# Optimization experiments

Measured on AMD Instinct MI355X. Metric: run time of the kernel, lower is better.

Reference implementation:

```python
import jax, jax.numpy as jnp
import numpy as np

SRC_V, TGT_V, EMB, ENC_H, DEC_H = 36616, 23262, 300, 512, 1024
T_SRC, T_TGT, B = 50, 50, 64


def setup_inputs():
    key = jax.random.key(0)
    ks = jax.random.split(key, 24)
    p = lambda k, s: jax.random.normal(k, s, dtype=jnp.float32) * 0.05
    return {
        'train_src_batch': jax.random.randint(ks[0], (T_SRC, B), 0, SRC_V),
        'train_trg_batch': jax.random.randint(ks[1], (T_TGT, B), 0, TGT_V),
        'enc_Wih_f': p(ks[2], (4 * ENC_H, EMB)), 'enc_Whh_f': p(ks[3], (4 * ENC_H, ENC_H)),
        'enc_bih_f': p(ks[4], (4 * ENC_H,)), 'enc_bhh_f': p(ks[5], (4 * ENC_H,)),
        'enc_Wih_r': p(ks[6], (4 * ENC_H, EMB)), 'enc_Whh_r': p(ks[7], (4 * ENC_H, ENC_H)),
        'enc_bih_r': p(ks[8], (4 * ENC_H,)), 'enc_bhh_r': p(ks[9], (4 * ENC_H,)),
        'dec_Wih': p(ks[10], (4 * DEC_H, DEC_H + EMB)), 'dec_Whh': p(ks[11], (4 * DEC_H, DEC_H)),
        'dec_bih': p(ks[12], (4 * DEC_H,)), 'dec_bhh': p(ks[13], (4 * DEC_H,)),
        'enc_emb': p(ks[14], (SRC_V, EMB)), 'dec_emb': p(ks[15], (TGT_V, EMB)),
        'wi': p(ks[16], (DEC_H, DEC_H)), 'wo': p(ks[17], (DEC_H, 2 * DEC_H)),
        'gen_w': p(ks[18], (TGT_V, DEC_H)), 'gen_b': p(ks[19], (TGT_V,)),
    }


def _lstm_update(gates, c):
    # PyTorch gate order: i, f, g, o
    i, f, g, o = jnp.split(gates, 4, axis=-1)
    c = jax.nn.sigmoid(f) * c + jax.nn.sigmoid(i) * jnp.tanh(g)
    h = jax.nn.sigmoid(o) * jnp.tanh(c)
    return h, c


def _run_lstm(x, Wih, Whh, bih, bhh, H):
    # x: [T, B, E]; precompute input projection for all timesteps
    xp = jnp.einsum('tbe,ge->tbg', x, Wih) + bih + bhh
    b = x.shape[1]
    def step(carry, xpt):
        h, c = carry
        h, c = _lstm_update(xpt + h @ Whh.T, c)
        return (h, c), h
    init = (jnp.zeros((b, H), x.dtype), jnp.zeros((b, H), x.dtype))
    (hT, cT), hs = jax.lax.scan(step, init, xp)
    return hs, hT, cT


def _forward(train_src_batch, train_trg_batch, enc_Wih_f, enc_Whh_f, enc_bih_f, enc_bhh_f,
             enc_Wih_r, enc_Whh_r, enc_bih_r, enc_bhh_r, dec_Wih, dec_Whh, dec_bih, dec_bhh,
             enc_emb, dec_emb, wi, wo, gen_w, gen_b):
    x = enc_emb[train_src_batch]                       # [T_src, B, 300]
    hs_f, hT_f, cT_f = _run_lstm(x, enc_Wih_f, enc_Whh_f, enc_bih_f, enc_bhh_f, ENC_H)
    hs_r, hT_r, cT_r = _run_lstm(x[::-1], enc_Wih_r, enc_Whh_r, enc_bih_r, enc_bhh_r, ENC_H)
    enc_out = jnp.concatenate([hs_f, hs_r[::-1]], axis=-1)  # [T_src, B, 1024]
    b = x.shape[1]
    # h.permute(1,2,0).view(B,1024): interleave fwd/bwd along last axis
    h0 = jnp.stack([hT_f, hT_r], axis=-1).reshape(b, DEC_H)
    c0 = jnp.stack([cT_f, cT_r], axis=-1).reshape(b, DEC_H)
    prev_emb = dec_emb[train_trg_batch[:-1]]           # teacher forcing: [T_tgt-1, B, 300]

    def dec_step(carry, pe):
        h, c = carry
        q = h @ wi.T                                   # [B, 1024]
        score = jnp.einsum('tbh,bh->tb', enc_out, q)   # [T_src, B]
        attn = jax.nn.softmax(score, axis=0)           # softmax over source time
        st = jnp.einsum('tb,tbh->bh', attn, enc_out)   # [B, 1024]
        ct = jnp.tanh(jnp.concatenate([st, h], axis=1) @ wo.T)
        inp = jnp.concatenate([ct, pe], axis=1)        # [B, 1324]
        gates = inp @ dec_Wih.T + h @ dec_Whh.T + dec_bih + dec_bhh
        h, c = _lstm_update(gates, c)
        logp = jax.nn.log_softmax(h @ gen_w.T + gen_b, axis=-1)
        return (h, c), logp

    _, outs = jax.lax.scan(dec_step, (h0, c0), prev_emb)  # [T_tgt-1, B, V]
    result = jnp.concatenate([jnp.zeros((1, b, TGT_V), outs.dtype), outs], axis=0)
    return result


def reference(train_src_batch, train_trg_batch, enc_Wih_f, enc_Whh_f, enc_bih_f, enc_bhh_f,
              enc_Wih_r, enc_Whh_r, enc_bih_r, enc_bhh_r, dec_Wih, dec_Whh, dec_bih, dec_bhh,
              enc_emb, dec_emb, wi, wo, gen_w, gen_b):
    return _forward(train_src_batch, train_trg_batch, enc_Wih_f, enc_Whh_f, enc_bih_f, enc_bhh_f,
                    enc_Wih_r, enc_Whh_r, enc_bih_r, enc_bhh_r, dec_Wih, dec_Whh, dec_bih, dec_bhh,
                    enc_emb, dec_emb, wi, wo, gen_w, gen_b)
```

## Files before the change

kernel.cpp:

```cpp
#include <hip/hip_runtime.h>
#include <cstdint>
#include <cmath>

#define NB    64
#define EMBD  300
#define EMBP  320
#define EH    512
#define DH    1024
#define GV    23262
#define GVP   23296
#define TSRC  50
#define TDEC  49
#define LDS_SCR 131072
#define LDS_TOT (131072 + 16384 + 256)
#define LDS_ENC (65536 + 16384 + 256)
#define FS    32

typedef __attribute__((ext_vector_type(8))) _Float16 f16x8;
typedef __attribute__((ext_vector_type(4))) float f32x4;

__device__ __forceinline__ float sigm(float x){ return 1.f/(1.f+expf(-x)); }

__device__ __forceinline__ void cohS16(_Float16* p, _Float16 v){
  union { _Float16 f; unsigned short u; } c; c.f = v;
  __hip_atomic_store((unsigned short*)p, c.u, __ATOMIC_RELAXED, __HIP_MEMORY_SCOPE_AGENT);
}
__device__ __forceinline__ void cohS32(float* p, float v){
  __hip_atomic_store(p, v, __ATOMIC_RELAXED, __HIP_MEMORY_SCOPE_AGENT);
}
__device__ __forceinline__ void cohS64(void* p, unsigned long long v){
  __hip_atomic_store((unsigned long long*)p, v, __ATOMIC_RELAXED, __HIP_MEMORY_SCOPE_AGENT);
}
__device__ __forceinline__ void cohS32u(void* p, unsigned int v){
  __hip_atomic_store((unsigned int*)p, v, __ATOMIC_RELAXED, __HIP_MEMORY_SCOPE_AGENT);
}
__device__ __forceinline__ unsigned short h2u(float f){
  union { _Float16 h; unsigned short u; } c; c.h = (_Float16)f; return c.u;
}
__device__ __forceinline__ unsigned long long pk4h(float a, float b, float c, float d){
  return (unsigned long long)h2u(a) | ((unsigned long long)h2u(b)<<16)
       | ((unsigned long long)h2u(c)<<32) | ((unsigned long long)h2u(d)<<48);
}
__device__ __forceinline__ unsigned int pk2h(float a, float b){
  return (unsigned int)h2u(a) | ((unsigned int)h2u(b)<<16);
}
__device__ __forceinline__ unsigned long long pk2f(float a, float b){
  union { float f; unsigned int u; } x, y; x.f = a; y.f = b;
  return (unsigned long long)x.u | ((unsigned long long)y.u<<32);
}

__device__ __forceinline__ int ldF(int* p){
  return __hip_atomic_load(p, __ATOMIC_RELAXED, __HIP_MEMORY_SCOPE_AGENT);
}
__device__ __forceinline__ void stF(int* p, int v){
  __hip_atomic_store(p, v, __ATOMIC_RELAXED, __HIP_MEMORY_SCOPE_AGENT);
}
__device__ __forceinline__ void post(int* flagArr, int idx, int epoch){
  __syncthreads();
  if (threadIdx.x == 0) stF(flagArr + idx*FS, epoch);
}
__device__ __forceinline__ void flagWaitIdx(int* flagArr, int myIdx, bool active, int epoch)
{
  if (active) {
    int* p = flagArr + myIdx*FS;
    while (ldF(p) < epoch) __builtin_amdgcn_s_sleep(1);
  }
  __syncthreads();
  __atomic_signal_fence(__ATOMIC_SEQ_CST);
}

__device__ __forceinline__ void stageW(char* dst, const _Float16* __restrict__ src,
                                       int srcld, int nrows, int ncols, int tid)
{
  const int nch = ncols >> 3;
  for (int i = tid; i < nrows*nch; i += 256) {
    int row = i / nch, c = i - row*nch;
    *(f16x8*)(dst + row*ncols*2 + ((c*16) ^ ((row&7)<<4))) =
        *(const f16x8*)(src + (size_t)row*srcld + c*8);
  }
}

template<int K>
__device__ __forceinline__ void mm16L(f32x4 (&acc)[4],
    const _Float16* __restrict__ A, int lda,
    const char* ldsB, int rowbytes, int koffB, int lane)
{
  const int r = lane & 15, q = lane >> 4;
  const _Float16* a0 = A + r*lda + q*8;
  const char* b0 = ldsB + r*rowbytes + koffB;
  const int sw = (r & 7) << 4;
#pragma unroll
  for (int g = 0; g < K/256; ++g) {
    f16x8 av[8][4], bv[8];
#pragma unroll
    for (int s = 0; s < 8; ++s) {
      int sl = g*8 + s;
      bv[s] = *(const f16x8*)(b0 + ((sl*64 + q*16) ^ sw));
#pragma unroll
      for (int m = 0; m < 4; ++m)
        av[s][m] = *(const f16x8*)(a0 + m*16*lda + sl*32);
    }
#pragma unroll
    for (int s = 0; s < 8; ++s)
#pragma unroll
      for (int m = 0; m < 4; ++m)
        acc[m] = __builtin_amdgcn_mfma_f32_16x16x32_f16(av[s][m], bv[s], acc[m], 0, 0, 0);
  }
}

__global__ void cvt16s(const float* __restrict__ src, _Float16* __restrict__ dst,
                       int rows, int sld, int scols, int dcols)
{
  int idx = blockIdx.x*256 + threadIdx.x;
  if (idx >= rows*dcols) return;
  int c = idx % dcols, rr = idx / dcols;
  dst[idx] = (c < scols) ? (_Float16)src[(size_t)rr*sld + c] : (_Float16)0.f;
}

__global__ void cvt16t(const float* __restrict__ src, _Float16* __restrict__ dst, int n)
{
  int idx = blockIdx.x*256 + threadIdx.x;
  if (idx >= n*n) return;
  int rr = idx / n, c = idx - rr*n;
  dst[(size_t)c*n + rr] = (_Float16)src[idx];
}

__global__ void addb(const float* __restrict__ a, const float* __restrict__ b,
                     float* __restrict__ o, int n)
{
  int i = blockIdx.x*256 + threadIdx.x;
  if (i < n) o[i] = a[i] + b[i];
}

__global__ void k_embed(const int* __restrict__ src, const int* __restrict__ trg,
                        const float* __restrict__ eemb, const float* __restrict__ demb,
                        _Float16* __restrict__ x_h, _Float16* __restrict__ xrev_h,
                        _Float16* __restrict__ pe_h)
{
  int idx = blockIdx.x*256 + threadIdx.x;
  const int tot1 = TSRC*NB*EMBP;
  const int tot2 = TDEC*NB*EMBP;
  if (idx < tot1) {
    int e = idx % EMBP, rb = idx / EMBP;
    int t = rb >> 6, b = rb & 63;
    float v = 0.f;
    if (e < EMBD) v = eemb[(size_t)src[rb]*EMBD + e];
    _Float16 hv = (_Float16)v;
    x_h[idx] = hv;
    xrev_h[(size_t)((TSRC-1-t)*NB + b)*EMBP + e] = hv;
  } else if (idx < tot1 + tot2) {
    int k = idx - tot1;
    int e = k % EMBP, rb = k / EMBP;
    float v = 0.f;
    if (e < EMBD) v = demb[(size_t)trg[rb]*EMBD + e];
    pe_h[k] = (_Float16)v;
  }
}

__device__ __forceinline__ void swz_block(int& m0, int& n0)
{
  int nwg = gridDim.x*gridDim.y;
  int flat = blockIdx.y*gridDim.x + blockIdx.x;
  int q = nwg >> 3, rr = nwg & 7;
  int xcd = flat & 7, pos = flat >> 3;
  int wg = (xcd < rr) ? xcd*(q+1) + pos : rr*(q+1) + (xcd-rr)*q + pos;
  m0 = (wg / gridDim.x) * 128;
  n0 = (wg % gridDim.x) * 128;
}

__global__ __launch_bounds__(256) void gemm128(
    const _Float16* __restrict__ A, int lda,
    const _Float16* __restrict__ W, int ldw,
    const float* __restrict__ bias,
    float* __restrict__ out, int ldo,
    int K, int mvalid, int nvalid, int rowoff)
{
  __shared__ _Float16 As[128*64];
  __shared__ _Float16 Bs[128*64];
  const int tid = threadIdx.x;
  int m0, n0;
  swz_block(m0, n0);
  const int w = tid >> 6, lane = tid & 63, r = lane & 15, q = lane >> 4;
  const int mw = (w >> 1)*64, nw = (w & 1)*64;
  f32x4 acc[4][4];
#pragma unroll
  for (int mi=0; mi<4; ++mi)
#pragma unroll
    for (int ni=0; ni<4; ++ni) acc[mi][ni] = 0.f;

  for (int kt = 0; kt < K; kt += 64) {
    f16x8 ra[4], rb[4];
#pragma unroll
    for (int j = 0; j < 4; ++j) {
      int c = j*256 + tid, row = c >> 3, cc = c & 7;
      ra[j] = *(const f16x8*)(A + (size_t)(m0+row)*lda + kt + cc*8);
      rb[j] = *(const f16x8*)(W + (size_t)(n0+row)*ldw + kt + cc*8);
    }
    __syncthreads();
#pragma unroll
    for (int j = 0; j < 4; ++j) {
      int c = j*256 + tid, row = c >> 3, cc = c & 7;
      int sw = cc ^ (row & 7);
      *(f16x8*)((char*)As + row*128 + (sw<<4)) = ra[j];
      *(f16x8*)((char*)Bs + row*128 + (sw<<4)) = rb[j];
    }
    __syncthreads();
#pragma unroll
    for (int kk = 0; kk < 64; kk += 32) {
      int ch = (kk >> 3) + q;
      f16x8 av[4], bv[4];
#pragma unroll
      for (int mi=0; mi<4; ++mi) {
        int row = mw + mi*16 + r;
        av[mi] = *(const f16x8*)((char*)As + row*128 + ((ch ^ (row&7))<<4));
      }
#pragma unroll
      for (int ni=0; ni<4; ++ni) {
        int row = nw + ni*16 + r;
        bv[ni] = *(const f16x8*)((char*)Bs + row*128 + ((ch ^ (row&7))<<4));
      }
#pragma unroll
      for (int mi=0; mi<4; ++mi)
#pragma unroll
        for (int ni=0; ni<4; ++ni)
          acc[mi][ni] = __builtin_amdgcn_mfma_f32_16x16x32_f16(av[mi], bv[ni], acc[mi][ni], 0,0,0);
    }
  }
#pragma unroll
  for (int mi=0; mi<4; ++mi)
#pragma unroll
    for (int ni=0; ni<4; ++ni)
#pragma unroll
      for (int e=0; e<4; ++e) {
        int mrow = m0 + mw + mi*16 + q*4 + e;
        int col  = n0 + nw + ni*16 + r;
        if (mrow < mvalid && col < nvalid)
          out[(size_t)(mrow + rowoff)*ldo + col] = acc[mi][ni][e] + bias[col];
      }
}

__global__ __launch_bounds__(256) void gemm128h(
    const _Float16* __restrict__ A, int lda,
    const _Float16* __restrict__ W, int ldw,
    const float* __restrict__ bias,
    _Float16* __restrict__ out, int ldo,
    int K, int mvalid, int nvalid)
{
  __shared__ _Float16 As[128*64];
  __shared__ _Float16 Bs[128*64];
  const int tid = threadIdx.x;
  int m0, n0;
  swz_block(m0, n0);
  const int w = tid >> 6, lane = tid & 63, r = lane & 15, q = lane >> 4;
  const int mw = (w >> 1)*64, nw = (w & 1)*64;
  f32x4 acc[4][4];
#pragma unroll
  for (int mi=0; mi<4; ++mi)
#pragma unroll
    for (int ni=0; ni<4; ++ni) acc[mi][ni] = 0.f;

  for (int kt = 0; kt < K; kt += 64) {
    f16x8 ra[4], rb[4];
#pragma unroll
    for (int j = 0; j < 4; ++j) {
      int c = j*256 + tid, row = c >> 3, cc = c & 7;
      ra[j] = *(const f16x8*)(A + (size_t)(m0+row)*lda + kt + cc*8);
      rb[j] = *(const f16x8*)(W + (size_t)(n0+row)*ldw + kt + cc*8);
    }
    __syncthreads();
#pragma unroll
    for (int j = 0; j < 4; ++j) {
      int c = j*256 + tid, row = c >> 3, cc = c & 7;
      int sw = cc ^ (row & 7);
      *(f16x8*)((char*)As + row*128 + (sw<<4)) = ra[j];
      *(f16x8*)((char*)Bs + row*128 + (sw<<4)) = rb[j];
    }
    __syncthreads();
#pragma unroll
    for (int kk = 0; kk < 64; kk += 32) {
      int ch = (kk >> 3) + q;
      f16x8 av[4], bv[4];
#pragma unroll
      for (int mi=0; mi<4; ++mi) {
        int row = mw + mi*16 + r;
        av[mi] = *(const f16x8*)((char*)As + row*128 + ((ch ^ (row&7))<<4));
      }
#pragma unroll
      for (int ni=0; ni<4; ++ni) {
        int row = nw + ni*16 + r;
        bv[ni] = *(const f16x8*)((char*)Bs + row*128 + ((ch ^ (row&7))<<4));
      }
#pragma unroll
      for (int mi=0; mi<4; ++mi)
#pragma unroll
        for (int ni=0; ni<4; ++ni)
          acc[mi][ni] = __builtin_amdgcn_mfma_f32_16x16x32_f16(av[mi], bv[ni], acc[mi][ni], 0,0,0);
    }
  }
#pragma unroll
  for (int mi=0; mi<4; ++mi)
#pragma unroll
    for (int ni=0; ni<4; ++ni)
#pragma unroll
      for (int e=0; e<4; ++e) {
        int mrow = m0 + mw + mi*16 + q*4 + e;
        int col  = n0 + nw + ni*16 + r;
        if (mrow < mvalid && col < nvalid)
          out[(size_t)mrow*ldo + col] = (_Float16)(acc[mi][ni][e] + bias[col]);
      }
}

struct EA {
  const _Float16 *whhF, *whhR;
  const float *xpF, *xpR;
  _Float16 *h;
  _Float16 *enc_out;
  _Float16 *dh0;
  float *dc;
  int *flags;
};

__global__ __launch_bounds__(256, 1) void enc_seq(EA a)
{
  extern __shared__ char lds[];
  const int tid = threadIdx.x, w = tid >> 6, lane = tid & 63;
  const int wgid = blockIdx.x;
  const int r = lane & 15, q4 = lane >> 4;
  float (*sm4)[64][16] = (float(*)[64][16])(lds + 65536);

  const int dir = wgid >> 5, j0 = (wgid & 31) << 4;
  const _Float16* whh = dir ? a.whhR : a.whhF;
  for (int g = 0; g < 4; ++g)
    stageW(lds + g*16384, whh + (size_t)(g*EH + j0)*EH, EH, 16, 512, tid);
  __syncthreads();

  const int b = tid >> 2, jq = (tid & 3) * 4;
  float creg[4] = {0.f, 0.f, 0.f, 0.f};
  const float* xpbase = dir ? a.xpR : a.xpF;

  for (int t = 0; t < TSRC; ++t) {
    float xr[4][4];
#pragma unroll
    for (int g = 0; g < 4; ++g)
#pragma unroll
      for (int k = 0; k < 4; ++k)
        xr[g][k] = xpbase[((size_t)t*NB + b)*2048 + g*EH + j0 + jq + k];
    if (t) flagWaitIdx(a.flags, dir*32 + tid, tid < 32, t);
    const _Float16* H = a.h + ((size_t)(TSRC-t)*2 + dir)*NB*EH;
    f32x4 acc[4];
#pragma unroll
    for (int m=0;m<4;++m) acc[m] = 0.f;
    mm16L<EH>(acc, H, EH, lds + w*16384, 1024, 0, lane);
#pragma unroll
    for (int m=0;m<4;++m)
#pragma unroll
      for (int e=0;e<4;++e) sm4[w][m*16 + q4*4 + e][r] = acc[m][e];
    __syncthreads();
    _Float16* Ho = a.h + ((size_t)(TSRC-1-t)*2 + dir)*NB*EH;
    const int erow = dir ? (TSRC-1 - t) : t;
    float hv[4];
#pragma unroll
    for (int k = 0; k < 4; ++k) {
      int jj = jq + k;
      float gi = sm4[0][b][jj] + xr[0][k];
      float gf = sm4[1][b][jj] + xr[1][k];
      float gg = sm4[2][b][jj] + xr[2][k];
      float go = sm4[3][b][jj] + xr[3][k];
      float cn = sigm(gf)*creg[k] + sigm(gi)*tanhf(gg);
      creg[k] = cn;
      hv[k] = sigm(go)*tanhf(cn);
    }
    cohS64(Ho + b*EH + j0 + jq, pk4h(hv[0],hv[1],hv[2],hv[3]));
    cohS64(a.enc_out + ((size_t)erow*NB + b)*DH + dir*EH + j0 + jq, pk4h(hv[0],hv[1],hv[2],hv[3]));
    if (t == TSRC-1) {
#pragma unroll
      for (int k = 0; k < 4; ++k) {
        int j = j0 + jq + k;
        cohS16(a.dh0 + b*DH + 2*j + dir, (_Float16)hv[k]);
        cohS32(a.dc + b*DH + 2*j + dir, creg[k]);
      }
    }
    post(a.flags, wgid, t+1);
  }
}

struct DA {
  const _Float16 *wo;
  const _Float16 *wdh;
  const _Float16 *w3c;
  const _Float16 *eq;
  const _Float16 *eo2;
  const _Float16 *pp;
  _Float16 *dh;
  float *dc;
  _Float16 *ct;
  float *wdd;
  _Float16 *hdec;
  int *flags;
};

__global__ __launch_bounds__(256, 1) void dec_seq(DA a)
{
  extern __shared__ char lds[];
  const int tid = threadIdx.x, w = tid >> 6, lane = tid & 63;
  const int wgid = blockIdx.x;
  const int r = lane & 15, q4 = lane >> 4;
  float (*sm4)[64][16] = (float(*)[64][16])(lds + LDS_SCR);
  float* qs = (float*)(lds + LDS_SCR);
  float* sc = (float*)(lds + LDS_SCR + 16384);

  int* FB  = a.flags;
  int* FCP = FB + 64*FS;
  int* FD  = FCP + 32*FS;

  if (wgid >= 64 && wgid < 96) {
    stageW(lds, a.wo + (size_t)((wgid-64)*32)*2048 + 1024, 2048, 32, 1024, tid);
  } else if (wgid >= 96) {
    int i = wgid - 96;
    for (int g = 0; g < 4; ++g)
      stageW(lds + g*8*2048, a.wdh + (size_t)(g*1024 + i*8)*DH, DH, 8, 1024, tid);
    for (int g = 0; g < 4; ++g)
      stageW(lds + 65536 + g*8*2048, a.w3c + (size_t)(g*1024 + i*8)*DH, DH, 8, 1024, tid);
  }
  __syncthreads();

  const bool isP2 = (wgid < 64);
  const bool isC  = (wgid >= 64 && wgid < 96);
  const bool isD  = (wgid >= 96);
  float dcreg[2] = {0.f, 0.f};

  for (int t = 0; t < TDEC; ++t) {
    const size_t cur = (size_t)(TDEC - t)*NB*DH;
    const size_t nxt = (size_t)(TDEC - 1 - t)*NB*DH;
    const _Float16* dhC = a.dh + cur;

    if (isC) {
      if (t) flagWaitIdx(FD, tid, tid < 128, t);
      const int col0 = (wgid - 64)*32;
      const int cs = w >> 1, kh = w & 1;
      f32x4 acc[4];
#pragma unroll
      for (int m=0;m<4;++m) acc[m] = 0.f;
      mm16L<512>(acc, dhC + kh*512, DH, lds + cs*16*2048, 2048, kh*1024, lane);
#pragma unroll
      for (int m=0;m<4;++m)
#pragma unroll
        for (int e=0;e<4;++e) sm4[w][m*16 + q4*4 + e][r] = acc[m][e];
      __syncthreads();
      for (int p = tid; p < 2048; p += 256) {
        int b = p >> 5, cc = p & 31;
        float v1, v2;
        int c1 = (cc & 30);
        v1 = sm4[((c1)>>4)*2][b][(c1)&15] + sm4[((c1)>>4)*2+1][b][(c1)&15];
        v2 = sm4[((c1+1)>>4)*2][b][(c1+1)&15] + sm4[((c1+1)>>4)*2+1][b][(c1+1)&15];
        if ((cc & 1) == 0)
          cohS64(a.wdd + cur + b*DH + col0 + c1, pk2f(v1, v2));
      }
      post(FCP, wgid - 64, t+1);
    }

    if (isP2) {
      if (t) flagWaitIdx(FD, tid, tid < 128, t);
      const int b = wgid;
      if (tid < 128) {
        f16x8 v = *(const f16x8*)(dhC + b*DH + tid*8);
#pragma unroll
        for (int k = 0; k < 8; ++k) qs[tid*8 + k] = (float)v[k];
      }
      __syncthreads();
      for (int tt = w; tt < TSRC; tt += 4) {
        const _Float16* er = a.eq + ((size_t)tt*NB + b)*DH + lane*16;
        const float* qq = qs + lane*16;
        f16x8 e0 = *(const f16x8*)(er);
        f16x8 e1 = *(const f16x8*)(er + 8);
        float s = 0.f;
#pragma unroll
        for (int ii=0; ii<8; ++ii) s += (float)e0[ii]*qq[ii];
#pragma unroll
        for (int ii=0; ii<8; ++ii) s += (float)e1[ii]*qq[8+ii];
#pragma unroll
        for (int o=32; o; o>>=1) s += __shfl_xor(s, o);
        if (lane == 0) sc[tt] = s;
      }
      __syncthreads();
      float mx = -1e30f;
      for (int tt=0; tt<TSRC; ++tt) mx = fmaxf(mx, sc[tt]);
      __syncthreads();
      if (tid < TSRC) sc[tid] = expf(sc[tid] - mx);
      __syncthreads();
      float s50 = 0.f;
      for (int tt=0; tt<TSRC; ++tt) s50 += sc[tt];
      const float inv = 1.f/s50;
      const int c0 = tid*4;
      float a0=0.f, a1=0.f, a2=0.f, a3=0.f;
      for (int tt=0; tt<TSRC; ++tt) {
        float wt = sc[tt];
        const _Float16* er = a.eo2 + ((size_t)tt*NB + b)*DH + c0;
        a0 += wt*(float)er[0]; a1 += wt*(float)er[1];
        a2 += wt*(float)er[2]; a3 += wt*(float)er[3];
      }
      flagWaitIdx(FCP, tid, tid < 32, t+1);
      f32x4 wd = *(const f32x4*)(a.wdd + cur + b*DH + c0);
      float v0 = tanhf(a0*inv + wd[0]);
      float v1 = tanhf(a1*inv + wd[1]);
      float v2 = tanhf(a2*inv + wd[2]);
      float v3 = tanhf(a3*inv + wd[3]);
      cohS64(a.ct + cur + b*DH + c0, pk4h(v0, v1, v2, v3));
      post(FB, wgid, t+1);
    }

    if (isD) {
      const int i = wgid - 96;
      if (t) flagWaitIdx(FD, tid, tid < 128, t);
      const int b = tid >> 2, j0 = i*8, jj2 = (tid & 3)*2;
      if (t == 0) {
        dcreg[0] = a.dc[b*DH + j0 + jj2];
        dcreg[1] = a.dc[b*DH + j0 + jj2 + 1];
      }
      const int cs = w >> 1, kh = w & 1;
      f32x4 acc[4];
#pragma unroll
      for (int m=0;m<4;++m) acc[m] = 0.f;
      mm16L<512>(acc, dhC + kh*512, DH, lds + cs*16*2048, 2048, kh*1024, lane);
      float ppv[4][2];
#pragma unroll
      for (int g = 0; g < 4; ++g)
#pragma unroll
        for (int k = 0; k < 2; ++k)
          ppv[g][k] = (float)a.pp[((size_t)t*NB + b)*4096 + g*DH + j0 + jj2 + k];
      flagWaitIdx(FB, tid, tid < 64, t+1);
      mm16L<512>(acc, a.ct + cur + kh*512, DH, lds + 65536 + cs*16*2048, 2048, kh*1024, lane);
#pragma unroll
      for (int m=0;m<4;++m)
#pragma unroll
        for (int e=0;e<4;++e) sm4[w][m*16 + q4*4 + e][r] = acc[m][e];
      __syncthreads();
      float hv[2];
#pragma unroll
      for (int k = 0; k < 2; ++k) {
        int jj = jj2 + k;
        float gi = sm4[0][b][jj]   + sm4[1][b][jj]   + ppv[0][k];
        float gf = sm4[0][b][8+jj] + sm4[1][b][8+jj] + ppv[1][k];
        float gg = sm4[2][b][jj]   + sm4[3][b][jj]   + ppv[2][k];
        float go = sm4[2][b][8+jj] + sm4[3][b][8+jj] + ppv[3][k];
        float cn = sigm(gf)*dcreg[k] + sigm(gi)*tanhf(gg);
        dcreg[k] = cn;
        hv[k] = sigm(go)*tanhf(cn);
      }
      cohS32u(a.dh + nxt + b*DH + j0 + jj2, pk2h(hv[0], hv[1]));
      post(FD, i, t+1);
      *(unsigned int*)(a.hdec + ((size_t)t*NB + b)*DH + j0 + jj2) = pk2h(hv[0], hv[1]);
    }
  }
}

__global__ __launch_bounds__(256) void lsm(float* __restrict__ out)
{
  const int row = NB + blockIdx.x;
  float* p = out + (size_t)row*GV;
  const int tid = threadIdx.x;
  __shared__ float rm[4], rl[4];
  float m = -1e30f, l = 0.f;
  for (int i = tid; i < GV; i += 256) {
    float v = p[i];
    float M = fmaxf(m, v);
    l = l*expf(m - M) + expf(v - M);
    m = M;
  }
  for (int off=32; off; off>>=1) {
    float m2 = __shfl_down(m, off), l2 = __shfl_down(l, off);
    float M = fmaxf(m, m2);
    l = l*expf(m - M) + l2*expf(m2 - M);
    m = M;
  }
  if ((tid & 63) == 0) { rm[tid>>6] = m; rl[tid>>6] = l; }
  __syncthreads();
  m = rm[0]; l = rl[0];
#pragma unroll
  for (int k=1; k<4; ++k) {
    float M = fmaxf(m, rm[k]);
    l = l*expf(m - M) + rl[k]*expf(rm[k] - M);
    m = M;
  }
  float lse = m + logf(l);
  for (int i = tid; i < GV; i += 256) p[i] -= lse;
}

extern "C" void kernel_launch(void* const* d_in, const int* in_sizes, int n_in,
                              void* d_out, int out_size, void* d_ws, size_t ws_size,
                              hipStream_t stream)
{
  const int*   src  = (const int*)d_in[0];
  const int*   trg  = (const int*)d_in[1];
  const float* WihF = (const float*)d_in[2];
  const float* WhhF = (const float*)d_in[3];
  const float* bihF = (const float*)d_in[4];
  const float* bhhF = (const float*)d_in[5];
  const float* WihR = (const float*)d_in[6];
  const float* WhhR = (const float*)d_in[7];
  const float* bihR = (const float*)d_in[8];
  const float* bhhR = (const float*)d_in[9];
  const float* dWih = (const float*)d_in[10];
  const float* dWhh = (const float*)d_in[11];
  const float* dbih = (const float*)d_in[12];
  const float* dbhh = (const float*)d_in[13];
  const float* eemb = (const float*)d_in[14];
  const float* demb = (const float*)d_in[15];
  const float* wi   = (const float*)d_in[16];
  const float* wo   = (const float*)d_in[17];
  const float* genw = (const float*)d_in[18];
  const float* genb = (const float*)d_in[19];
  float* out = (float*)d_out;

  char* ws = (char*)d_ws;
  size_t off = 0;
  auto alloc = [&](size_t bytes)->char* {
    char* p = ws + off; off = (off + bytes + 255) & ~(size_t)255; return p;
  };
  _Float16* x_h    = (_Float16*)alloc((size_t)TSRC*NB*EMBP*2);
  _Float16* xrev_h = (_Float16*)alloc((size_t)TSRC*NB*EMBP*2);
  _Float16* pe_h   = (_Float16*)alloc((size_t)TDEC*NB*EMBP*2);
  _Float16* wihF_h = (_Float16*)alloc((size_t)2048*EMBP*2);
  _Float16* wihR_h = (_Float16*)alloc((size_t)2048*EMBP*2);
  _Float16* whhF_h = (_Float16*)alloc((size_t)2048*EH*2);
  _Float16* whhR_h = (_Float16*)alloc((size_t)2048*EH*2);
  _Float16* wdh_h  = (_Float16*)alloc((size_t)4096*DH*2);
  _Float16* wo_h   = (_Float16*)alloc((size_t)DH*2048*2);
  _Float16* w3c    = (_Float16*)alloc((size_t)4096*DH*2);
  _Float16* w3pe   = (_Float16*)alloc((size_t)4096*EMBP*2);
  _Float16* wiT_h  = (_Float16*)alloc((size_t)DH*DH*2);
  _Float16* genw_h = (_Float16*)alloc((size_t)GVP*DH*2);
  float* b4f   = (float*)alloc(2048*4);
  float* b4r   = (float*)alloc(2048*4);
  float* db4   = (float*)alloc(4096*4);
  float* zb    = (float*)alloc(DH*4);
  float* xp_f  = (float*)alloc((size_t)TSRC*NB*2048*4);
  float* xp_r  = (float*)alloc((size_t)TSRC*NB*2048*4);
  _Float16* peproj = (_Float16*)alloc((size_t)TDEC*NB*4096*2);
  _Float16* enc_out = (_Float16*)alloc((size_t)TSRC*NB*DH*2);
  _Float16* eq_h  = (_Float16*)alloc((size_t)TSRC*NB*DH*2);
  _Float16* eo2_h = (_Float16*)alloc((size_t)TSRC*NB*DH*2);
  _Float16* hbuf = (_Float16*)alloc((size_t)(TSRC+1)*2*NB*EH*2);
  _Float16* dh = (_Float16*)alloc((size_t)(TDEC+1)*NB*DH*2);
  float* dc = (float*)alloc((size_t)NB*DH*4);
  _Float16* ct = (_Float16*)alloc((size_t)(TDEC+1)*NB*DH*2);
  float* wdd = (float*)alloc((size_t)(TDEC+1)*NB*DH*4);
  _Float16* hdec = (_Float16*)alloc((size_t)3200*DH*2);
  int* eflags = (int*)alloc(64*FS*4);
  int* dflags = (int*)alloc(224*FS*4);
  (void)in_sizes; (void)n_in; (void)out_size; (void)ws_size;

  hipMemsetAsync(hbuf + (size_t)TSRC*2*NB*EH, 0, (size_t)2*NB*EH*2, stream);
  hipMemsetAsync(hdec + (size_t)3136*DH, 0, (size_t)64*DH*2, stream);
  hipMemsetAsync(genw_h + (size_t)GV*DH, 0, (size_t)(GVP-GV)*DH*2, stream);
  hipMemsetAsync(out, 0, (size_t)NB*GV*4, stream);
  hipMemsetAsync(zb, 0, DH*4, stream);
  hipMemsetAsync(eflags, 0, 64*FS*4, stream);
  hipMemsetAsync(dflags, 0, 224*FS*4, stream);

  auto cgrid = [](size_t n){ return dim3((unsigned)((n + 255)/256)); };

  cvt16s<<<cgrid((size_t)2048*EMBP),256,0,stream>>>(WihF, wihF_h, 2048, EMBD, EMBD, EMBP);
  cvt16s<<<cgrid((size_t)2048*EMBP),256,0,stream>>>(WihR, wihR_h, 2048, EMBD, EMBD, EMBP);
  cvt16s<<<cgrid((size_t)2048*EH),256,0,stream>>>(WhhF, whhF_h, 2048, EH, EH, EH);
  cvt16s<<<cgrid((size_t)2048*EH),256,0,stream>>>(WhhR, whhR_h, 2048, EH, EH, EH);
  cvt16s<<<cgrid((size_t)4096*DH),256,0,stream>>>(dWhh, wdh_h, 4096, DH, DH, DH);
  cvt16s<<<cgrid((size_t)DH*2048),256,0,stream>>>(wo, wo_h, DH, 2048, 2048, 2048);
  cvt16s<<<cgrid((size_t)4096*DH),256,0,stream>>>(dWih, w3c, 4096, 1324, 1024, 1024);
  cvt16s<<<cgrid((size_t)4096*EMBP),256,0,stream>>>(dWih + 1024, w3pe, 4096, 1324, 300, EMBP);
  cvt16t<<<cgrid((size_t)DH*DH),256,0,stream>>>(wi, wiT_h, DH);
  cvt16s<<<cgrid((size_t)GV*DH),256,0,stream>>>(genw, genw_h, GV, DH, DH, DH);
  addb<<<cgrid(2048),256,0,stream>>>(bihF, bhhF, b4f, 2048);
  addb<<<cgrid(2048),256,0,stream>>>(bihR, bhhR, b4r, 2048);
  addb<<<cgrid(4096),256,0,stream>>>(dbih, dbhh, db4, 4096);
  k_embed<<<cgrid((size_t)(TSRC+TDEC)*NB*EMBP),256,0,stream>>>(src, trg, eemb, demb, x_h, xrev_h, pe_h);

  gemm128<<<dim3(16,25),256,0,stream>>>(x_h,    EMBP, wihF_h, EMBP, b4f, xp_f, 2048, EMBP, 3200, 2048, 0);
  gemm128<<<dim3(16,25),256,0,stream>>>(xrev_h, EMBP, wihR_h, EMBP, b4r, xp_r, 2048, EMBP, 3200, 2048, 0);
  gemm128h<<<dim3(32,25),256,0,stream>>>(pe_h, EMBP, w3pe, EMBP, db4, peproj, 4096, EMBP, 3136, 4096);

  EA ea;
  ea.whhF = whhF_h; ea.whhR = whhR_h;
  ea.xpF = xp_f; ea.xpR = xp_r;
  ea.h = hbuf; ea.enc_out = enc_out;
  ea.dh0 = dh + (size_t)TDEC*NB*DH;
  ea.dc = dc;
  ea.flags = eflags;
  hipFuncSetAttribute((const void*)enc_seq,
                      hipFuncAttributeMaxDynamicSharedMemorySize, LDS_ENC);
  enc_seq<<<dim3(64), 256, LDS_ENC, stream>>>(ea);

  gemm128h<<<dim3(8,25),256,0,stream>>>(enc_out, DH, wiT_h, DH, zb, eq_h, DH, DH, 3200, DH);
  gemm128h<<<dim3(8,25),256,0,stream>>>(enc_out, DH, wo_h, 2048, zb, eo2_h, DH, DH, 3200, DH);

  DA da;
  da.wo = wo_h; da.wdh = wdh_h; da.w3c = w3c;
  da.eq = eq_h; da.eo2 = eo2_h;
  da.pp = peproj;
  da.dh = dh; da.dc = dc;
  da.ct = ct; da.wdd = wdd;
  da.hdec = hdec;
  da.flags = dflags;
  hipFuncSetAttribute((const void*)dec_seq,
                      hipFuncAttributeMaxDynamicSharedMemorySize, LDS_TOT);
  dec_seq<<<dim3(224), 256, LDS_TOT, stream>>>(da);

  gemm128<<<dim3(GVP/128,25),256,0,stream>>>(hdec, DH, genw_h, DH, genb, out, GV, DH, 3136, GV, NB);
  lsm<<<3136,256,0,stream>>>(out);
}
```

Before: 2.255 ms.

## Fuse log-softmax row stats into generator GEMM and use direct global-to-LDS loads

The generator GEMM epilogue now computes a per-row online max and sum-exp over each 128-column tile and writes them to a small stats buffer. The log-softmax kernel then merges 182 partial stats per row instead of re-reading the full 23262-wide logits row to find them, which removes one full pass over the logits. Separately, both GEMM kernels stage A and W tiles with global_load_lds (buffer-to-LDS) instead of going through registers, and add an extra barrier per k-step. The epilogue adds extra exp work and shuffles in the GEMM.

```diff
diff --git a/kernel.cpp b/kernel.cpp
--- a/kernel.cpp
+++ b/kernel.cpp
@@ -9,6 +9,7 @@
 #define DH    1024
 #define GV    23262
 #define GVP   23296
+#define NCB   182
 #define TSRC  50
 #define TDEC  49
 #define LDS_SCR 131072
@@ -18,6 +19,9 @@
 
 typedef __attribute__((ext_vector_type(8))) _Float16 f16x8;
 typedef __attribute__((ext_vector_type(4))) float f32x4;
+
+typedef __attribute__((address_space(1))) const void gas_t;
+typedef __attribute__((address_space(3))) void las_t;
 
 __device__ __forceinline__ float sigm(float x){ return 1.f/(1.f+expf(-x)); }
 
@@ -168,12 +172,31 @@
   n0 = (wg % gridDim.x) * 128;
 }
 
+__device__ __forceinline__ void stage_glds(const _Float16* __restrict__ A, int lda, int m0,
+                                           const _Float16* __restrict__ W, int ldw, int n0,
+                                           int kt, char* As, char* Bs, int tid)
+{
+#pragma unroll
+  for (int j = 0; j < 4; ++j) {
+    int idx = j*256 + tid;
+    int row = idx >> 3, cc = idx & 7;
+    int sc = cc ^ (row & 7);
+    __builtin_amdgcn_global_load_lds(
+        (gas_t*)(A + (size_t)(m0+row)*lda + kt + sc*8),
+        (las_t*)(As + (j*256 + (tid & 0xffc0))*16), 16, 0, 0);
+    __builtin_amdgcn_global_load_lds(
+        (gas_t*)(W + (size_t)(n0+row)*ldw + kt + sc*8),
+        (las_t*)(Bs + (j*256 + (tid & 0xffc0))*16), 16, 0, 0);
+  }
+}
+
 __global__ __launch_bounds__(256) void gemm128(
     const _Float16* __restrict__ A, int lda,
     const _Float16* __restrict__ W, int ldw,
     const float* __restrict__ bias,
     float* __restrict__ out, int ldo,
-    int K, int mvalid, int nvalid, int rowoff)
+    int K, int mvalid, int nvalid, int rowoff,
+    float* __restrict__ gstats)
 {
   __shared__ _Float16 As[128*64];
   __shared__ _Float16 Bs[128*64];
@@ -189,21 +212,7 @@
     for (int ni=0; ni<4; ++ni) acc[mi][ni] = 0.f;
 
   for (int kt = 0; kt < K; kt += 64) {
-    f16x8 ra[4], rb[4];
-#pragma unroll
-    for (int j = 0; j < 4; ++j) {
-      int c = j*256 + tid, row = c >> 3, cc = c & 7;
-      ra[j] = *(const f16x8*)(A + (size_t)(m0+row)*lda + kt + cc*8);
-      rb[j] = *(const f16x8*)(W + (size_t)(n0+row)*ldw + kt + cc*8);
-    }
-    __syncthreads();
-#pragma unroll
-    for (int j = 0; j < 4; ++j) {
-      int c = j*256 + tid, row = c >> 3, cc = c & 7;
-      int sw = cc ^ (row & 7);
-      *(f16x8*)((char*)As + row*128 + (sw<<4)) = ra[j];
-      *(f16x8*)((char*)Bs + row*128 + (sw<<4)) = rb[j];
-    }
+    stage_glds(A, lda, m0, W, ldw, n0, kt, (char*)As, (char*)Bs, tid);
     __syncthreads();
 #pragma unroll
     for (int kk = 0; kk < 64; kk += 32) {
@@ -225,6 +234,7 @@
         for (int ni=0; ni<4; ++ni)
           acc[mi][ni] = __builtin_amdgcn_mfma_f32_16x16x32_f16(av[mi], bv[ni], acc[mi][ni], 0,0,0);
     }
+    __syncthreads();
   }
 #pragma unroll
   for (int mi=0; mi<4; ++mi)
@@ -237,6 +247,66 @@
         if (mrow < mvalid && col < nvalid)
           out[(size_t)(mrow + rowoff)*ldo + col] = acc[mi][ni][e] + bias[col];
       }
+
+  if (gstats) {
+    float pm[4][4], pl[4][4];
+#pragma unroll
+    for (int mi=0;mi<4;++mi)
+#pragma unroll
+      for (int e=0;e<4;++e){ pm[mi][e] = -1e30f; pl[mi][e] = 0.f; }
+#pragma unroll
+    for (int mi=0;mi<4;++mi)
+#pragma unroll
+      for (int ni=0;ni<4;++ni)
+#pragma unroll
+        for (int e=0;e<4;++e) {
+          int col = n0 + nw + ni*16 + r;
+          if (col < nvalid) {
+            float v = acc[mi][ni][e] + bias[col];
+            float M = fmaxf(pm[mi][e], v);
+            pl[mi][e] = pl[mi][e]*expf(pm[mi][e]-M) + expf(v-M);
+            pm[mi][e] = M;
+          }
+        }
+#pragma unroll
+    for (int o=1;o<16;o<<=1)
+#pragma unroll
+      for (int mi=0;mi<4;++mi)
+#pragma unroll
+        for (int e=0;e<4;++e) {
+          float m2 = __shfl_xor(pm[mi][e], o);
+          float l2 = __shfl_xor(pl[mi][e], o);
+          float M = fmaxf(pm[mi][e], m2);
+          pl[mi][e] = pl[mi][e]*expf(pm[mi][e]-M) + l2*expf(m2-M);
+          pm[mi][e] = M;
+        }
+    __syncthreads();
+    float* sred = (float*)As;
+    if (r == 0) {
+#pragma unroll
+      for (int mi=0;mi<4;++mi)
+#pragma unroll
+        for (int e=0;e<4;++e) {
+          int rowl = mi*16 + q*4 + e;
+          sred[(w*64 + rowl)*2 + 0] = pm[mi][e];
+          sred[(w*64 + rowl)*2 + 1] = pl[mi][e];
+        }
+    }
+    __syncthreads();
+    if (tid < 128) {
+      int half = tid >> 6, rowl = tid & 63;
+      int wA = half*2, wB = half*2 + 1;
+      float mA = sred[(wA*64+rowl)*2], lA = sred[(wA*64+rowl)*2+1];
+      float mB = sred[(wB*64+rowl)*2], lB = sred[(wB*64+rowl)*2+1];
+      float M = fmaxf(mA, mB);
+      float L = lA*expf(mA-M) + lB*expf(mB-M);
+      int mrow = m0 + half*64 + rowl;
+      if (mrow < mvalid) {
+        float* gp = gstats + ((size_t)mrow*NCB + (n0 >> 7))*2;
+        gp[0] = M; gp[1] = L;
+      }
+    }
+  }
 }
 
 __global__ __launch_bounds__(256) void gemm128h(
@@ -260,21 +330,7 @@
     for (int ni=0; ni<4; ++ni) acc[mi][ni] = 0.f;
 
   for (int kt = 0; kt < K; kt += 64) {
-    f16x8 ra[4], rb[4];
-#pragma unroll
-    for (int j = 0; j < 4; ++j) {
-      int c = j*256 + tid, row = c >> 3, cc = c & 7;
-      ra[j] = *(const f16x8*)(A + (size_t)(m0+row)*lda + kt + cc*8);
-      rb[j] = *(const f16x8*)(W + (size_t)(n0+row)*ldw + kt + cc*8);
-    }
-    __syncthreads();
-#pragma unroll
-    for (int j = 0; j < 4; ++j) {
-      int c = j*256 + tid, row = c >> 3, cc = c & 7;
-      int sw = cc ^ (row & 7);
-      *(f16x8*)((char*)As + row*128 + (sw<<4)) = ra[j];
-      *(f16x8*)((char*)Bs + row*128 + (sw<<4)) = rb[j];
-    }
+    stage_glds(A, lda, m0, W, ldw, n0, kt, (char*)As, (char*)Bs, tid);
     __syncthreads();
 #pragma unroll
     for (int kk = 0; kk < 64; kk += 32) {
@@ -296,6 +352,7 @@
         for (int ni=0; ni<4; ++ni)
           acc[mi][ni] = __builtin_amdgcn_mfma_f32_16x16x32_f16(av[mi], bv[ni], acc[mi][ni], 0,0,0);
     }
+    __syncthreads();
   }
 #pragma unroll
   for (int mi=0; mi<4; ++mi)
@@ -554,21 +611,20 @@
   }
 }
 
-__global__ __launch_bounds__(256) void lsm(float* __restrict__ out)
-{
-  const int row = NB + blockIdx.x;
-  float* p = out + (size_t)row*GV;
+__global__ __launch_bounds__(256) void lsm(const float* __restrict__ gstats,
+                                           float* __restrict__ out)
+{
+  const int row = blockIdx.x;
+  float* p = out + (size_t)(row + NB)*GV;
   const int tid = threadIdx.x;
   __shared__ float rm[4], rl[4];
   float m = -1e30f, l = 0.f;
-  for (int i = tid; i < GV; i += 256) {
-    float v = p[i];
-    float M = fmaxf(m, v);
-    l = l*expf(m - M) + expf(v - M);
-    m = M;
-  }
-  for (int off=32; off; off>>=1) {
-    float m2 = __shfl_down(m, off), l2 = __shfl_down(l, off);
+  if (tid < NCB) {
+    const float* gp = gstats + ((size_t)row*NCB + tid)*2;
+    m = gp[0]; l = gp[1];
+  }
+  for (int o=32; o; o>>=1) {
+    float m2 = __shfl_down(m, o), l2 = __shfl_down(l, o);
     float M = fmaxf(m, m2);
     l = l*expf(m - M) + l2*expf(m2 - M);
     m = M;
@@ -646,6 +702,7 @@
   _Float16* ct = (_Float16*)alloc((size_t)(TDEC+1)*NB*DH*2);
   float* wdd = (float*)alloc((size_t)(TDEC+1)*NB*DH*4);
   _Float16* hdec = (_Float16*)alloc((size_t)3200*DH*2);
+  float* gstats = (float*)alloc((size_t)3136*NCB*2*4);
   int* eflags = (int*)alloc(64*FS*4);
   int* dflags = (int*)alloc(224*FS*4);
   (void)in_sizes; (void)n_in; (void)out_size; (void)ws_size;
@@ -675,8 +732,8 @@
   addb<<<cgrid(4096),256,0,stream>>>(dbih, dbhh, db4, 4096);
   k_embed<<<cgrid((size_t)(TSRC+TDEC)*NB*EMBP),256,0,stream>>>(src, trg, eemb, demb, x_h, xrev_h, pe_h);
 
-  gemm128<<<dim3(16,25),256,0,stream>>>(x_h,    EMBP, wihF_h, EMBP, b4f, xp_f, 2048, EMBP, 3200, 2048, 0);
-  gemm128<<<dim3(16,25),256,0,stream>>>(xrev_h, EMBP, wihR_h, EMBP, b4r, xp_r, 2048, EMBP, 3200, 2048, 0);
+  gemm128<<<dim3(16,25),256,0,stream>>>(x_h,    EMBP, wihF_h, EMBP, b4f, xp_f, 2048, EMBP, 3200, 2048, 0, nullptr);
+  gemm128<<<dim3(16,25),256,0,stream>>>(xrev_h, EMBP, wihR_h, EMBP, b4r, xp_r, 2048, EMBP, 3200, 2048, 0, nullptr);
   gemm128h<<<dim3(32,25),256,0,stream>>>(pe_h, EMBP, w3pe, EMBP, db4, peproj, 4096, EMBP, 3136, 4096);
 
   EA ea;
@@ -705,6 +762,6 @@
                       hipFuncAttributeMaxDynamicSharedMemorySize, LDS_TOT);
   dec_seq<<<dim3(224), 256, LDS_TOT, stream>>>(da);
 
-  gemm128<<<dim3(GVP/128,25),256,0,stream>>>(hdec, DH, genw_h, DH, genb, out, GV, DH, 3136, GV, NB);
-  lsm<<<3136,256,0,stream>>>(out);
-}
+  gemm128<<<dim3(GVP/128,25),256,0,stream>>>(hdec, DH, genw_h, DH, genb, out, GV, DH, 3136, GV, NB, gstats);
+  lsm<<<3136,256,0,stream>>>(gstats, out);
+}
```

After: 2.305 ms. 1.02x slower.
